# Optimization experiments

Hardware: AMD Instinct MI355X
Metric: run time of the kernel (lower is better)

The kernel has to match this reference:

```python
import jax, jax.numpy as jnp
import numpy as np

N, D, E, H, K = 4096, 512, 32, 128, 4  # tokens, d_model, n_experts, expert hidden, top-k


def setup_inputs() -> dict:
    key = jax.random.key(0)
    k0, k1, k2, k3 = jax.random.split(key, 4)
    x = jax.random.normal(k0, (N, D), dtype=jnp.float32)
    # router weights, init std = d**-0.5 (matches get_initializer std)
    expert_sel = jax.random.normal(k1, (E, D), dtype=jnp.float32) * (D ** -0.5)
    # per-expert MLP weights (Linear stores [out, in]; we keep [E, in, out] layout)
    w1 = jax.random.normal(k2, (E, D, H), dtype=jnp.float32) * (D ** -0.5)
    w2 = jax.random.normal(k3, (E, H, D), dtype=jnp.float32) * (H ** -0.5)
    return {"x": x, "expert_sel": expert_sel, "w1": w1, "w2": w2}


def reference(x, expert_sel, w1, w2):
    # routing: sigmoid selection, top-k experts per token
    scores = jax.nn.sigmoid(x @ expert_sel.T)          # [N, E]
    gate_vals, gate_idx = jax.lax.top_k(scores, K)     # [N, K]
    # dense gate matrix with only top-k nonzero (sparse dispatch/combine weights)
    gate = (jax.nn.one_hot(gate_idx, E, dtype=x.dtype) * gate_vals[..., None]).sum(-2)  # [N, E]
    # per-expert MLP; gating at hidden is exact since experts have no bias:
    # gate * (relu(x W1) W2) == (gate * relu(x W1)) W2
    h = jax.nn.relu(jnp.einsum('nd,edh->neh', x, w1)) * gate[..., None]  # [N, E, H]
    y = jnp.einsum('neh,ehv->nv', h, w2)               # [N, D]
    return y
```

## Files before the change

### kernel.cpp

```cpp
#include <hip/hip_runtime.h>
#include <hip/hip_bf16.h>

#define NTOK 4096
#define DM   512
#define NE   32
#define HD   128
#define TK   4
#define NRB  1024

typedef unsigned short u16;
typedef unsigned int   u32;
typedef u16   u16x4 __attribute__((ext_vector_type(4)));
typedef u16   u16x8 __attribute__((ext_vector_type(8)));
typedef short short8 __attribute__((ext_vector_type(8)));
typedef float f32x4 __attribute__((ext_vector_type(4)));
typedef int   int4v __attribute__((ext_vector_type(4)));

__device__ __forceinline__ u16 f2bf(float f) {
    union { float f; u32 u; } v; v.f = f;
    return (u16)((v.u + 0x7FFFu + ((v.u >> 16) & 1u)) >> 16);
}
__device__ __forceinline__ float bf2f(u16 h) {
    union { u32 u; float f; } v; v.u = ((u32)h) << 16; return v.f;
}

__global__ __launch_bounds__(256) void prep_kernel(const float* __restrict__ x,
                                                   const float* __restrict__ sel,
                                                   const float* __restrict__ w1,
                                                   const float* __restrict__ w2,
                                                   int* __restrict__ blk_cnt,
                                                   int* __restrict__ tok_list,
                                                   float* __restrict__ gate_list,
                                                   u16* __restrict__ xbf,
                                                   u16* __restrict__ wf1,
                                                   u16* __restrict__ wf2) {
    __shared__ float  xs[4][520];
    __shared__ double sc[4][33];
    __shared__ int    pk_e[16];
    __shared__ float  pk_g[16];
    int tid = threadIdx.x;
    int wv = tid >> 6, lane = tid & 63;

    if (blockIdx.x >= NRB) {
        int m = lane & 15, q = lane >> 4;
        int f0 = ((blockIdx.x - NRB) * 4 + wv) * 2;
        const float* in[2]; u16* outp[2]; int Nd[2];
#pragma unroll
        for (int u = 0; u < 2; ++u) {
            int w = f0 + u;
            if (w < 4096) {
                int e = w >> 7, rem = w & 127, ks = rem >> 3, nt = rem & 7;
                in[u] = w1 + (size_t)e * DM * HD + (size_t)(32 * ks + q * 8) * HD + 16 * nt + m;
                Nd[u] = HD;
                outp[u] = wf1 + (size_t)w * 512 + lane * 8;
            } else {
                int wl = w - 4096, e = wl >> 7, rem = wl & 127, ks = rem >> 5, nt = rem & 31;
                in[u] = w2 + (size_t)e * HD * DM + (size_t)(32 * ks + q * 8) * DM + 16 * nt + m;
                Nd[u] = DM;
                outp[u] = wf2 + (size_t)wl * 512 + lane * 8;
            }
        }
        float v[2][8];
#pragma unroll
        for (int u = 0; u < 2; ++u)
#pragma unroll
            for (int j = 0; j < 8; ++j) v[u][j] = in[u][(size_t)j * Nd[u]];
#pragma unroll
        for (int u = 0; u < 2; ++u) {
            u16x8 h;
#pragma unroll
            for (int j = 0; j < 8; ++j) h[j] = f2bf(v[u][j]);
            *(u16x8*)outp[u] = h;
        }
        return;
    }

    int bl = blockIdx.x;
    int tb = bl * 4;
#pragma unroll
    for (int rep = 0; rep < 2; ++rep) {
        int idx = (rep * 256 + tid) * 4;
        int row = idx >> 9, col = idx & 511;
        f32x4 v = *(const f32x4*)(x + (size_t)(tb + row) * DM + col);
        *(f32x4*)&xs[row][col] = v;
        u16x4 h;
#pragma unroll
        for (int j = 0; j < 4; ++j) h[j] = f2bf(v[j]);
        *(u16x4*)(xbf + (size_t)(tb + row) * DM + col) = h;
    }
    __syncthreads();

    int tok = tid & 3, seg = (tid >> 2) & 1, e = tid >> 3;
    const float* sp = sel + (size_t)e * DM + seg * 256;
    const float* xp = &xs[tok][seg * 256];
    double pa = 0.0, pb = 0.0, pc = 0.0, pd = 0.0;
#pragma unroll 4
    for (int j = 0; j < 256; j += 16) {
        f32x4 x0 = *(const f32x4*)(xp + j);
        f32x4 x1 = *(const f32x4*)(xp + j + 4);
        f32x4 x2 = *(const f32x4*)(xp + j + 8);
        f32x4 x3 = *(const f32x4*)(xp + j + 12);
        f32x4 s0 = *(const f32x4*)(sp + j);
        f32x4 s1 = *(const f32x4*)(sp + j + 4);
        f32x4 s2 = *(const f32x4*)(sp + j + 8);
        f32x4 s3 = *(const f32x4*)(sp + j + 12);
#pragma unroll
        for (int k = 0; k < 4; ++k) {
            pa = fma((double)x0[k], (double)s0[k], pa);
            pb = fma((double)x1[k], (double)s1[k], pb);
            pc = fma((double)x2[k], (double)s2[k], pc);
            pd = fma((double)x3[k], (double)s3[k], pd);
        }
    }
    double p = (pa + pb) + (pc + pd);
    p += __shfl_xor(p, 4);
    if (seg == 0) sc[tok][e] = p;
    __syncthreads();

    if (tid < 4) {
        unsigned mask = 0;
        for (int k = 0; k < TK; ++k) {
            double best = -1e300; int be = 0;
            for (int ee = 0; ee < NE; ++ee) {
                double v = sc[tid][ee];
                if (!((mask >> ee) & 1u) && v > best) { best = v; be = ee; }
            }
            mask |= 1u << be;
            pk_e[tid * 4 + k] = be;
            pk_g[tid * 4 + k] = 1.0f / (1.0f + __expf(-(float)best));
        }
    }
    __syncthreads();

    if (tid < NE) {
        int e2 = tid, cnt = 0;
        int base = (e2 * NRB + bl) * 4;
#pragma unroll
        for (int i = 0; i < 16; ++i) {
            if (pk_e[i] == e2) {
                tok_list[base + cnt]  = ((i & 3) << 16) | (tb + (i >> 2));
                gate_list[base + cnt] = pk_g[i];
                ++cnt;
            }
        }
        blk_cnt[e2 * NRB + bl] = cnt;
    }
}

__global__ __launch_bounds__(256, 2) void moe_mlp_kernel(const u16* __restrict__ xbf,
                                                         const u16* __restrict__ wf1,
                                                         const u16* __restrict__ wf2,
                                                         const int* __restrict__ blk_cnt,
                                                         const int* __restrict__ tok_list,
                                                         const float* __restrict__ gate_list,
                                                         u16* __restrict__ part,
                                                         float* __restrict__ out,
                                                         int use_part) {
    __shared__ int   s_tot[4];
    __shared__ int   s_red[4][4];
    __shared__ int   s_pref[NRB + 1];
    __shared__ int   s_ent[32];
    __shared__ float s_gate[32];
    __shared__ __align__(16) u16 Hm[32][136];
    __shared__ __align__(16) u16 Ct[32][520];

    int tid = threadIdx.x;
    int wv = tid >> 6, lane = tid & 63;
    int xcd = blockIdx.x & 7, idx0 = blockIdx.x >> 3;

    int lsums[4];
#pragma unroll
    for (int j = 0; j < 4; ++j) {
        int4v v = *(const int4v*)&blk_cnt[(size_t)(xcd + 8 * j) * NRB + tid * 4];
        lsums[j] = v[0] + v[1] + v[2] + v[3];
    }
#pragma unroll
    for (int j = 0; j < 4; ++j) {
        int s = lsums[j];
#pragma unroll
        for (int off = 32; off >= 1; off >>= 1) s += __shfl_down(s, off);
        if (lane == 0) s_red[wv][j] = s;
    }
    __syncthreads();
    if (tid < 4) s_tot[tid] = s_red[0][tid] + s_red[1][tid] + s_red[2][tid] + s_red[3][tid];
    __syncthreads();

    int c0 = s_tot[0], c1 = s_tot[1], c2 = s_tot[2], c3 = s_tot[3];
    int n0 = (c0 + 31) >> 5, n1 = (c1 + 31) >> 5, n2 = (c2 + 31) >> 5, n3 = (c3 + 31) >> 5;
    int tot = n0 + n1 + n2 + n3;

    int m = lane & 15, q = lane >> 4;
    int r = wv >> 1, c = wv & 1;
    int e_last = -1;

    for (int idx = idx0; idx < tot; idx += 128) {
        int e2, t2, cc;
        if (idx < n0)                { e2 = xcd;      t2 = idx;                cc = c0; }
        else if (idx < n0 + n1)      { e2 = xcd + 8;  t2 = idx - n0;           cc = c1; }
        else if (idx < n0 + n1 + n2) { e2 = xcd + 16; t2 = idx - n0 - n1;      cc = c2; }
        else                         { e2 = xcd + 24; t2 = idx - n0 - n1 - n2; cc = c3; }
        int rows = cc - t2 * 32; if (rows > 32) rows = 32;

        __syncthreads();

        if (e2 != e_last) {
            int4v v = *(const int4v*)&blk_cnt[(size_t)e2 * NRB + tid * 4];
            int lsum = v[0] + v[1] + v[2] + v[3];
            int incl = lsum;
#pragma unroll
            for (int off = 1; off < 64; off <<= 1) {
                int t3 = __shfl_up(incl, off);
                if (lane >= off) incl += t3;
            }
            if (lane == 63) s_red[0][wv] = incl;
            __syncthreads();
            int woff = 0;
#pragma unroll
            for (int w2 = 0; w2 < 4; ++w2) if (w2 < wv) woff += s_red[0][w2];
            int excl = woff + incl - lsum;
            s_pref[tid * 4 + 0] = excl;
            s_pref[tid * 4 + 1] = excl + v[0];
            s_pref[tid * 4 + 2] = excl + v[0] + v[1];
            s_pref[tid * 4 + 3] = excl + v[0] + v[1] + v[2];
            if (tid == 255) s_pref[NRB] = excl + lsum;
            e_last = e2;
            __syncthreads();
        }

        if (tid < 32) {
            int row = t2 * 32 + tid;
            bool val = tid < rows;
            int rr = val ? row : 0;
            int lo = 0, hi = NRB;
            while (hi - lo > 1) { int mid = (lo + hi) >> 1; if (s_pref[mid] <= rr) lo = mid; else hi = mid; }
            int sub = rr - s_pref[lo];
            s_ent[tid]  = tok_list[((size_t)e2 * NRB + lo) * 4 + sub];
            s_gate[tid] = val ? gate_list[((size_t)e2 * NRB + lo) * 4 + sub] : 0.0f;
        }
        __syncthreads();

        const u16* w1f = wf1 + (size_t)e2 * (128 * 512);
        const u16* w2f = wf2 + (size_t)e2 * (128 * 512);
        const u16* a0 = xbf + (size_t)(s_ent[16 * r + m] & 0xFFFF) * DM + q * 8;

        short8 ab[2][2];
        short8 bb[2][2][4];
#pragma unroll
        for (int kk = 0; kk < 2; ++kk) {
            ab[0][kk] = *(const short8*)(a0 + 32 * kk);
            const u16* bp = w1f + (size_t)kk * 4096 + (size_t)(4 * c) * 512 + lane * 8;
#pragma unroll
            for (int n = 0; n < 4; ++n) bb[0][kk][n] = *(const short8*)(bp + n * 512);
        }
        f32x4 acc[4];
#pragma unroll
        for (int n = 0; n < 4; ++n) acc[n] = (f32x4){0.f, 0.f, 0.f, 0.f};

#pragma unroll
        for (int kp = 0; kp < 8; ++kp) {
            int cur = kp & 1, nxt = cur ^ 1;
            if (kp < 7) {
                int ks0 = 2 * (kp + 1);
#pragma unroll
                for (int kk = 0; kk < 2; ++kk) {
                    ab[nxt][kk] = *(const short8*)(a0 + 32 * (ks0 + kk));
                    const u16* bp = w1f + (size_t)(ks0 + kk) * 4096 + (size_t)(4 * c) * 512 + lane * 8;
#pragma unroll
                    for (int n = 0; n < 4; ++n) bb[nxt][kk][n] = *(const short8*)(bp + n * 512);
                }
            }
#pragma unroll
            for (int kk = 0; kk < 2; ++kk)
#pragma unroll
                for (int n = 0; n < 4; ++n)
                    acc[n] = __builtin_amdgcn_mfma_f32_16x16x32_bf16(ab[cur][kk],
                                                                     bb[cur][kk][n],
                                                                     acc[n], 0, 0, 0);
        }

        {
            int rb = 16 * r + q * 4;
#pragma unroll
            for (int n = 0; n < 4; ++n)
#pragma unroll
                for (int rr2 = 0; rr2 < 4; ++rr2)
                    Hm[rb + rr2][64 * c + 16 * n + m] =
                        f2bf(fmaxf(acc[n][rr2], 0.f) * s_gate[rb + rr2]);
        }

        short8 cb[2][8];
        {
            const u16* bp = w2f + (size_t)(wv * 8) * 512 + lane * 8;
#pragma unroll
            for (int n = 0; n < 8; ++n) cb[0][n] = *(const short8*)(bp + n * 512);
        }
        __syncthreads();

        f32x4 acc2[2][8];
#pragma unroll
        for (int i = 0; i < 2; ++i)
#pragma unroll
            for (int n = 0; n < 8; ++n) acc2[i][n] = (f32x4){0.f, 0.f, 0.f, 0.f};
#pragma unroll
        for (int ks = 0; ks < 4; ++ks) {
            int cur = ks & 1, nxt = cur ^ 1;
            if (ks < 3) {
                const u16* bp = w2f + (size_t)((ks + 1) * 32 + wv * 8) * 512 + lane * 8;
#pragma unroll
                for (int n = 0; n < 8; ++n) cb[nxt][n] = *(const short8*)(bp + n * 512);
            }
            short8 h0 = *(const short8*)&Hm[m][32 * ks + q * 8];
            short8 h1 = *(const short8*)&Hm[16 + m][32 * ks + q * 8];
#pragma unroll
            for (int n = 0; n < 8; ++n) {
                acc2[0][n] = __builtin_amdgcn_mfma_f32_16x16x32_bf16(h0, cb[cur][n], acc2[0][n], 0, 0, 0);
                acc2[1][n] = __builtin_amdgcn_mfma_f32_16x16x32_bf16(h1, cb[cur][n], acc2[1][n], 0, 0, 0);
            }
        }

#pragma unroll
        for (int i = 0; i < 2; ++i) {
            int rb = 16 * i + q * 4;
#pragma unroll
            for (int n = 0; n < 8; ++n)
#pragma unroll
                for (int rr2 = 0; rr2 < 4; ++rr2)
                    Ct[rb + rr2][128 * wv + 16 * n + m] = f2bf(acc2[i][n][rr2]);
        }
        __syncthreads();
#pragma unroll
        for (int rep = 0; rep < 8; ++rep) {
            int rl = rep * 4 + wv;
            u16x8 v = *(const u16x8*)&Ct[rl][lane * 8];
            if (rl < rows) {
                int en = s_ent[rl];
                int tk = en & 0xFFFF, sl2 = en >> 16;
                if (use_part) {
                    *(u16x8*)(part + ((size_t)sl2 * NTOK + tk) * DM + lane * 8) = v;
                } else {
                    float* op = out + (size_t)tk * DM + lane * 8;
#pragma unroll
                    for (int j = 0; j < 8; ++j) atomicAdd(&op[j], bf2f(v[j]));
                }
            }
        }
    }
}

__global__ __launch_bounds__(256) void combine_kernel(const u16* __restrict__ part,
                                                      float* __restrict__ out) {
    size_t off = ((size_t)blockIdx.x * 256 + threadIdx.x) * 8;
    float s[8] = {0, 0, 0, 0, 0, 0, 0, 0};
#pragma unroll
    for (int k = 0; k < TK; ++k) {
        u16x8 p = *(const u16x8*)(part + (size_t)k * NTOK * DM + off);
#pragma unroll
        for (int j = 0; j < 8; ++j) s[j] += bf2f(p[j]);
    }
    *(f32x4*)(out + off)     = (f32x4){s[0], s[1], s[2], s[3]};
    *(f32x4*)(out + off + 4) = (f32x4){s[4], s[5], s[6], s[7]};
}

extern "C" void kernel_launch(void* const* d_in, const int* in_sizes, int n_in,
                              void* d_out, int out_size, void* d_ws, size_t ws_size,
                              hipStream_t stream) {
    (void)in_sizes; (void)n_in; (void)out_size;
    const float* x   = (const float*)d_in[0];
    const float* sel = (const float*)d_in[1];
    const float* w1  = (const float*)d_in[2];
    const float* w2  = (const float*)d_in[3];
    float* out = (float*)d_out;

    char* ws = (char*)d_ws;
    int*   blk_cnt   = (int*)(ws);
    int*   tok_list  = (int*)(ws + (size_t)NE * NRB * 4);
    float* gate_list = (float*)(ws + (size_t)NE * NRB * 4 * 5);
    u16*   xbf  = (u16*)(ws + (size_t)NE * NRB * 4 * 9);
    u16*   wf1  = xbf + (size_t)NTOK * DM;
    u16*   wf2  = wf1 + (size_t)NE * HD * DM;
    u16*   part = wf2 + (size_t)NE * HD * DM;

    size_t need = (size_t)NE * NRB * 4 * 9 + (size_t)NTOK * DM * 2
                + 2 * (size_t)NE * HD * DM * 2 + (size_t)TK * NTOK * DM * 2;
    int use_part = (ws_size >= need) ? 1 : 0;

    if (!use_part)
        hipMemsetAsync(d_out, 0, (size_t)NTOK * DM * sizeof(float), stream);

    prep_kernel<<<2048, 256, 0, stream>>>(x, sel, w1, w2, blk_cnt, tok_list,
                                          gate_list, xbf, wf1, wf2);
    moe_mlp_kernel<<<1024, 256, 0, stream>>>(xbf, wf1, wf2, blk_cnt, tok_list,
                                             gate_list, part, out, use_part);
    if (use_part)
        combine_kernel<<<NTOK * DM / 8 / 256, 256, 0, stream>>>(part, out);
}
```

Measured before the change: 114.2 us.

## Fuse combine into MoE kernel via grid barrier and halve routing blocks

Removes the separate combine launch by adding a software grid-wide barrier at the end of the MoE MLP kernel, after which each of the 512 persistent blocks sums the four bf16 partial slices into the output. The routing prep now handles 8 tokens per block with full-length dot products, so blk_cnt and the prefix scan shrink to 512 entries. The MLP grid is halved to 512 blocks, each looping over twice as many tiles. This trades one kernel launch and shorter scans for a spin barrier that assumes all 512 blocks are co-resident, and for less parallelism in the main GEMM phase.

```diff
diff --git a/kernel.cpp b/kernel.cpp
--- a/kernel.cpp
+++ b/kernel.cpp
@@ -6,7 +6,9 @@
 #define NE   32
 #define HD   128
 #define TK   4
-#define NRB  1024
+#define RB   512
+#define SLOTW 32
+#define MGRID 512
 
 typedef unsigned short u16;
 typedef unsigned int   u32;
@@ -14,7 +16,7 @@
 typedef u16   u16x8 __attribute__((ext_vector_type(8)));
 typedef short short8 __attribute__((ext_vector_type(8)));
 typedef float f32x4 __attribute__((ext_vector_type(4)));
-typedef int   int4v __attribute__((ext_vector_type(4)));
+typedef int   int2v __attribute__((ext_vector_type(2)));
 
 __device__ __forceinline__ u16 f2bf(float f) {
     union { float f; u32 u; } v; v.f = f;
@@ -22,6 +24,16 @@
 }
 __device__ __forceinline__ float bf2f(u16 h) {
     union { u32 u; float f; } v; v.u = ((u32)h) << 16; return v.f;
+}
+
+__device__ __forceinline__ void grid_sync(u32* bar, u32 target) {
+    __syncthreads();
+    if (threadIdx.x == 0) {
+        __hip_atomic_fetch_add(bar, 1u, __ATOMIC_ACQ_REL, __HIP_MEMORY_SCOPE_AGENT);
+        while (__hip_atomic_load(bar, __ATOMIC_ACQUIRE, __HIP_MEMORY_SCOPE_AGENT) < target)
+            __builtin_amdgcn_s_sleep(2);
+    }
+    __syncthreads();
 }
 
 __global__ __launch_bounds__(256) void prep_kernel(const float* __restrict__ x,
@@ -29,21 +41,24 @@
                                                    const float* __restrict__ w1,
                                                    const float* __restrict__ w2,
                                                    int* __restrict__ blk_cnt,
+                                                   u32* __restrict__ bar,
                                                    int* __restrict__ tok_list,
                                                    float* __restrict__ gate_list,
                                                    u16* __restrict__ xbf,
                                                    u16* __restrict__ wf1,
                                                    u16* __restrict__ wf2) {
-    __shared__ float  xs[4][520];
-    __shared__ double sc[4][33];
-    __shared__ int    pk_e[16];
-    __shared__ float  pk_g[16];
+    __shared__ __align__(16) float  xs[8][520];
+    __shared__ double sc[8][33];
+    __shared__ int    pk_e[32];
+    __shared__ float  pk_g[32];
     int tid = threadIdx.x;
     int wv = tid >> 6, lane = tid & 63;
 
-    if (blockIdx.x >= NRB) {
+    if (blockIdx.x == 0 && tid == 0) *bar = 0;
+
+    if (blockIdx.x >= RB) {
         int m = lane & 15, q = lane >> 4;
-        int f0 = ((blockIdx.x - NRB) * 4 + wv) * 2;
+        int f0 = ((blockIdx.x - RB) * 4 + wv) * 2;
         const float* in[2]; u16* outp[2]; int Nd[2];
 #pragma unroll
         for (int u = 0; u < 2; ++u) {
@@ -76,9 +91,9 @@
     }
 
     int bl = blockIdx.x;
-    int tb = bl * 4;
-#pragma unroll
-    for (int rep = 0; rep < 2; ++rep) {
+    int tb = bl * 8;
+#pragma unroll
+    for (int rep = 0; rep < 4; ++rep) {
         int idx = (rep * 256 + tid) * 4;
         int row = idx >> 9, col = idx & 511;
         f32x4 v = *(const f32x4*)(x + (size_t)(tb + row) * DM + col);
@@ -90,34 +105,34 @@
     }
     __syncthreads();
 
-    int tok = tid & 3, seg = (tid >> 2) & 1, e = tid >> 3;
-    const float* sp = sel + (size_t)e * DM + seg * 256;
-    const float* xp = &xs[tok][seg * 256];
-    double pa = 0.0, pb = 0.0, pc = 0.0, pd = 0.0;
+    {
+        int tok = tid & 7, e = tid >> 3;
+        const float* sp = sel + (size_t)e * DM;
+        const float* xp = xs[tok];
+        double pa = 0.0, pb = 0.0, pc = 0.0, pd = 0.0;
 #pragma unroll 4
-    for (int j = 0; j < 256; j += 16) {
-        f32x4 x0 = *(const f32x4*)(xp + j);
-        f32x4 x1 = *(const f32x4*)(xp + j + 4);
-        f32x4 x2 = *(const f32x4*)(xp + j + 8);
-        f32x4 x3 = *(const f32x4*)(xp + j + 12);
-        f32x4 s0 = *(const f32x4*)(sp + j);
-        f32x4 s1 = *(const f32x4*)(sp + j + 4);
-        f32x4 s2 = *(const f32x4*)(sp + j + 8);
-        f32x4 s3 = *(const f32x4*)(sp + j + 12);
-#pragma unroll
-        for (int k = 0; k < 4; ++k) {
-            pa = fma((double)x0[k], (double)s0[k], pa);
-            pb = fma((double)x1[k], (double)s1[k], pb);
-            pc = fma((double)x2[k], (double)s2[k], pc);
-            pd = fma((double)x3[k], (double)s3[k], pd);
-        }
-    }
-    double p = (pa + pb) + (pc + pd);
-    p += __shfl_xor(p, 4);
-    if (seg == 0) sc[tok][e] = p;
-    __syncthreads();
-
-    if (tid < 4) {
+        for (int j = 0; j < 512; j += 16) {
+            f32x4 x0 = *(const f32x4*)(xp + j);
+            f32x4 x1 = *(const f32x4*)(xp + j + 4);
+            f32x4 x2 = *(const f32x4*)(xp + j + 8);
+            f32x4 x3 = *(const f32x4*)(xp + j + 12);
+            f32x4 s0 = *(const f32x4*)(sp + j);
+            f32x4 s1 = *(const f32x4*)(sp + j + 4);
+            f32x4 s2 = *(const f32x4*)(sp + j + 8);
+            f32x4 s3 = *(const f32x4*)(sp + j + 12);
+#pragma unroll
+            for (int k = 0; k < 4; ++k) {
+                pa = fma((double)x0[k], (double)s0[k], pa);
+                pb = fma((double)x1[k], (double)s1[k], pb);
+                pc = fma((double)x2[k], (double)s2[k], pc);
+                pd = fma((double)x3[k], (double)s3[k], pd);
+            }
+        }
+        sc[tok][e] = (pa + pb) + (pc + pd);
+    }
+    __syncthreads();
+
+    if (tid < 8) {
         unsigned mask = 0;
         for (int k = 0; k < TK; ++k) {
             double best = -1e300; int be = 0;
@@ -134,16 +149,16 @@
 
     if (tid < NE) {
         int e2 = tid, cnt = 0;
-        int base = (e2 * NRB + bl) * 4;
-#pragma unroll
-        for (int i = 0; i < 16; ++i) {
+        int base = (e2 * RB + bl) * SLOTW;
+#pragma unroll
+        for (int i = 0; i < 32; ++i) {
             if (pk_e[i] == e2) {
                 tok_list[base + cnt]  = ((i & 3) << 16) | (tb + (i >> 2));
                 gate_list[base + cnt] = pk_g[i];
                 ++cnt;
             }
         }
-        blk_cnt[e2 * NRB + bl] = cnt;
+        blk_cnt[e2 * RB + bl] = cnt;
     }
 }
 
@@ -153,12 +168,13 @@
                                                          const int* __restrict__ blk_cnt,
                                                          const int* __restrict__ tok_list,
                                                          const float* __restrict__ gate_list,
+                                                         u32* __restrict__ bar,
                                                          u16* __restrict__ part,
                                                          float* __restrict__ out,
                                                          int use_part) {
     __shared__ int   s_tot[4];
     __shared__ int   s_red[4][4];
-    __shared__ int   s_pref[NRB + 1];
+    __shared__ int   s_pref[RB + 1];
     __shared__ int   s_ent[32];
     __shared__ float s_gate[32];
     __shared__ __align__(16) u16 Hm[32][136];
@@ -168,15 +184,10 @@
     int wv = tid >> 6, lane = tid & 63;
     int xcd = blockIdx.x & 7, idx0 = blockIdx.x >> 3;
 
-    int lsums[4];
 #pragma unroll
     for (int j = 0; j < 4; ++j) {
-        int4v v = *(const int4v*)&blk_cnt[(size_t)(xcd + 8 * j) * NRB + tid * 4];
-        lsums[j] = v[0] + v[1] + v[2] + v[3];
-    }
-#pragma unroll
-    for (int j = 0; j < 4; ++j) {
-        int s = lsums[j];
+        int2v v = *(const int2v*)&blk_cnt[(size_t)(xcd + 8 * j) * RB + tid * 2];
+        int s = v[0] + v[1];
 #pragma unroll
         for (int off = 32; off >= 1; off >>= 1) s += __shfl_down(s, off);
         if (lane == 0) s_red[wv][j] = s;
@@ -193,7 +204,7 @@
     int r = wv >> 1, c = wv & 1;
     int e_last = -1;
 
-    for (int idx = idx0; idx < tot; idx += 128) {
+    for (int idx = idx0; idx < tot; idx += 64) {
         int e2, t2, cc;
         if (idx < n0)                { e2 = xcd;      t2 = idx;                cc = c0; }
         else if (idx < n0 + n1)      { e2 = xcd + 8;  t2 = idx - n0;           cc = c1; }
@@ -204,8 +215,8 @@
         __syncthreads();
 
         if (e2 != e_last) {
-            int4v v = *(const int4v*)&blk_cnt[(size_t)e2 * NRB + tid * 4];
-            int lsum = v[0] + v[1] + v[2] + v[3];
+            int2v v = *(const int2v*)&blk_cnt[(size_t)e2 * RB + tid * 2];
+            int lsum = v[0] + v[1];
             int incl = lsum;
 #pragma unroll
             for (int off = 1; off < 64; off <<= 1) {
@@ -218,11 +229,9 @@
 #pragma unroll
             for (int w2 = 0; w2 < 4; ++w2) if (w2 < wv) woff += s_red[0][w2];
             int excl = woff + incl - lsum;
-            s_pref[tid * 4 + 0] = excl;
-            s_pref[tid * 4 + 1] = excl + v[0];
-            s_pref[tid * 4 + 2] = excl + v[0] + v[1];
-            s_pref[tid * 4 + 3] = excl + v[0] + v[1] + v[2];
-            if (tid == 255) s_pref[NRB] = excl + lsum;
+            s_pref[tid * 2 + 0] = excl;
+            s_pref[tid * 2 + 1] = excl + v[0];
+            if (tid == 255) s_pref[RB] = excl + lsum;
             e_last = e2;
             __syncthreads();
         }
@@ -231,11 +240,11 @@
             int row = t2 * 32 + tid;
             bool val = tid < rows;
             int rr = val ? row : 0;
-            int lo = 0, hi = NRB;
+            int lo = 0, hi = RB;
             while (hi - lo > 1) { int mid = (lo + hi) >> 1; if (s_pref[mid] <= rr) lo = mid; else hi = mid; }
             int sub = rr - s_pref[lo];
-            s_ent[tid]  = tok_list[((size_t)e2 * NRB + lo) * 4 + sub];
-            s_gate[tid] = val ? gate_list[((size_t)e2 * NRB + lo) * 4 + sub] : 0.0f;
+            s_ent[tid]  = tok_list[((size_t)e2 * RB + lo) * SLOTW + sub];
+            s_gate[tid] = val ? gate_list[((size_t)e2 * RB + lo) * SLOTW + sub] : 0.0f;
         }
         __syncthreads();
 
@@ -344,21 +353,26 @@
                 }
             }
         }
-    }
-}
-
-__global__ __launch_bounds__(256) void combine_kernel(const u16* __restrict__ part,
-                                                      float* __restrict__ out) {
-    size_t off = ((size_t)blockIdx.x * 256 + threadIdx.x) * 8;
-    float s[8] = {0, 0, 0, 0, 0, 0, 0, 0};
-#pragma unroll
-    for (int k = 0; k < TK; ++k) {
-        u16x8 p = *(const u16x8*)(part + (size_t)k * NTOK * DM + off);
-#pragma unroll
-        for (int j = 0; j < 8; ++j) s[j] += bf2f(p[j]);
-    }
-    *(f32x4*)(out + off)     = (f32x4){s[0], s[1], s[2], s[3]};
-    *(f32x4*)(out + off + 4) = (f32x4){s[4], s[5], s[6], s[7]};
+        __syncthreads();
+    }
+
+    if (!use_part) return;
+
+    grid_sync(bar, MGRID);
+
+#pragma unroll
+    for (int rep = 0; rep < 2; ++rep) {
+        size_t off = (((size_t)blockIdx.x + (size_t)rep * MGRID) * 256 + tid) * 8;
+        float s[8] = {0, 0, 0, 0, 0, 0, 0, 0};
+#pragma unroll
+        for (int k = 0; k < TK; ++k) {
+            u16x8 p = *(const u16x8*)(part + (size_t)k * NTOK * DM + off);
+#pragma unroll
+            for (int j = 0; j < 8; ++j) s[j] += bf2f(p[j]);
+        }
+        *(f32x4*)(out + off)     = (f32x4){s[0], s[1], s[2], s[3]};
+        *(f32x4*)(out + off + 4) = (f32x4){s[4], s[5], s[6], s[7]};
+    }
 }
 
 extern "C" void kernel_launch(void* const* d_in, const int* in_sizes, int n_in,
@@ -373,24 +387,24 @@
 
     char* ws = (char*)d_ws;
     int*   blk_cnt   = (int*)(ws);
-    int*   tok_list  = (int*)(ws + (size_t)NE * NRB * 4);
-    float* gate_list = (float*)(ws + (size_t)NE * NRB * 4 * 5);
-    u16*   xbf  = (u16*)(ws + (size_t)NE * NRB * 4 * 9);
+    u32*   bar       = (u32*)(ws + (size_t)NE * RB * 4);
+    int*   tok_list  = (int*)(ws + (size_t)NE * RB * 4 + 256);
+    float* gate_list = (float*)((char*)tok_list + (size_t)NE * RB * SLOTW * 4);
+    u16*   xbf  = (u16*)((char*)gate_list + (size_t)NE * RB * SLOTW * 4);
     u16*   wf1  = xbf + (size_t)NTOK * DM;
     u16*   wf2  = wf1 + (size_t)NE * HD * DM;
     u16*   part = wf2 + (size_t)NE * HD * DM;
 
-    size_t need = (size_t)NE * NRB * 4 * 9 + (size_t)NTOK * DM * 2
-                + 2 * (size_t)NE * HD * DM * 2 + (size_t)TK * NTOK * DM * 2;
+    size_t need = (size_t)NE * RB * 4 + 256 + 2 * (size_t)NE * RB * SLOTW * 4
+                + (size_t)NTOK * DM * 2 + 2 * (size_t)NE * HD * DM * 2
+                + (size_t)TK * NTOK * DM * 2;
     int use_part = (ws_size >= need) ? 1 : 0;
 
     if (!use_part)
         hipMemsetAsync(d_out, 0, (size_t)NTOK * DM * sizeof(float), stream);
 
-    prep_kernel<<<2048, 256, 0, stream>>>(x, sel, w1, w2, blk_cnt, tok_list,
+    prep_kernel<<<1536, 256, 0, stream>>>(x, sel, w1, w2, blk_cnt, bar, tok_list,
                                           gate_list, xbf, wf1, wf2);
-    moe_mlp_kernel<<<1024, 256, 0, stream>>>(xbf, wf1, wf2, blk_cnt, tok_list,
-                                             gate_list, part, out, use_part);
-    if (use_part)
-        combine_kernel<<<NTOK * DM / 8 / 256, 256, 0, stream>>>(part, out);
-}
+    moe_mlp_kernel<<<MGRID, 256, 0, stream>>>(xbf, wf1, wf2, blk_cnt, tok_list,
+                                              gate_list, bar, part, out, use_part);
+}
```

Measured after the change: 205.8 us. 1.8x slower.
